# Performance work log

Hardware: AMD Instinct MI355X
Metric: run time of the kernel (lower is better)

Reference implementation:

```python
import jax, jax.numpy as jnp
import numpy as np

DIM = 96
EPS = 1e-5

def setup_inputs() -> dict:
    key = jax.random.key(0)
    k1, k2, k3, k4 = jax.random.split(key, 4)
    x = jax.random.normal(k1, (2, DIM, 32, 64, 64), dtype=jnp.float32)
    # LayerNorm(8*dim) params and Linear(8*dim -> 2*dim, bias=False) weight
    gamma = jnp.ones((8 * DIM,), dtype=jnp.float32)
    beta = jnp.zeros((8 * DIM,), dtype=jnp.float32)
    w_red = jax.random.normal(k2, (8 * DIM, 2 * DIM), dtype=jnp.float32) * (1.0 / np.sqrt(8 * DIM))
    return {"x": x, "gamma": gamma, "beta": beta, "w_red": w_red}


def _patch_merge(x, gamma, beta, w_red):
    B, C, D, H, W = x.shape
    # pad trailing spatial dims to even (static shapes -> python ifs are fine)
    if (D % 2) or (H % 2) or (W % 2):
        x = jnp.pad(x, ((0, 0), (0, 0), (0, D % 2), (0, H % 2), (0, W % 2)))
    x = jnp.transpose(x, (0, 2, 3, 4, 1))  # B, D, H, W, C
    # gather the 8 octant sub-lattices and concat on channel
    parts = [x[:, d::2, h::2, w::2, :]
             for d in (0, 1) for h in (0, 1) for w in (0, 1)]
    # torch order: x0..x7 indexed by (d,h,w) bits with d slowest -> matches loop order
    y = jnp.concatenate(parts, axis=-1)  # B, D/2, H/2, W/2, 8C
    # LayerNorm over last dim
    mu = jnp.mean(y, axis=-1, keepdims=True)
    var = jnp.mean(jnp.square(y - mu), axis=-1, keepdims=True)
    y = (y - mu) * jax.lax.rsqrt(var + EPS) * gamma + beta
    # Linear 8C -> 2C, no bias
    y = jnp.einsum('bdhwc,co->bdhwo', y, w_red)
    return jnp.transpose(y, (0, 4, 1, 2, 3))  # B, 2C, D/2, H/2, W/2


def reference(x, gamma, beta, w_red):
    return _patch_merge(x, gamma, beta, w_red)
```

## Files before the change

kernel.cpp:

```cpp
#include <hip/hip_runtime.h>

typedef __attribute__((ext_vector_type(8))) short short8;
typedef __attribute__((ext_vector_type(4))) float float4v;

__device__ __forceinline__ unsigned short f2bf(float f) {
  unsigned int u = __float_as_uint(f);
  u += 0x7fffu + ((u >> 16) & 1u);
  return (unsigned short)(u >> 16);
}
__device__ __forceinline__ float bf2f(unsigned short h) {
  return __uint_as_float(((unsigned int)h) << 16);
}

__global__ __launch_bounds__(256)
void prep_kernel(const float* __restrict__ w_red, const float* __restrict__ gamma,
                 const float* __restrict__ beta, unsigned short* __restrict__ w_bf,
                 float* __restrict__ colsum, float* __restrict__ bias) {
  const int n = blockIdx.x;
  const int t = threadIdx.x;
  float cs = 0.f, bs = 0.f;
#pragma unroll
  for (int j = 0; j < 3; ++j) {
    int kp = j * 256 + t;
    int ko = (kp & 7) * 96 + (kp >> 3);
    float w = w_red[(size_t)ko * 192 + n];
    unsigned short v = f2bf(gamma[ko] * w);
    w_bf[(size_t)n * 768 + kp] = v;
    cs += bf2f(v);
    bs += beta[ko] * w;
  }
#pragma unroll
  for (int off = 1; off < 64; off <<= 1) {
    cs += __shfl_xor(cs, off, 64);
    bs += __shfl_xor(bs, off, 64);
  }
  __shared__ float red[2][4];
  const int wave = t >> 6;
  if ((t & 63) == 0) { red[0][wave] = cs; red[1][wave] = bs; }
  __syncthreads();
  if (t == 0) {
    colsum[n] = red[0][0] + red[0][1] + red[0][2] + red[0][3];
    bias[n]   = red[1][0] + red[1][1] + red[1][2] + red[1][3];
  }
}

__global__ __launch_bounds__(256, 3)
void pm_kernel(const float* __restrict__ x, const unsigned short* __restrict__ w_bf,
               const float* __restrict__ colsum, const float* __restrict__ bias,
               float* __restrict__ out) {
  __shared__ __align__(16) unsigned short Y[32][776];
  __shared__ float4 part4[4][16];
  __shared__ float smu[32], srs[32];

  const int tid = threadIdx.x;
  const int bid = blockIdx.x;
  const int b  = bid >> 9;
  const int dz = (bid >> 5) & 15;
  const int hy = bid & 31;

  const float* xb = x + (size_t)b * 12582912u + (size_t)dz * 8192u + (size_t)hy * 128u;

  float sum0 = 0.f, sq0 = 0.f, sum1 = 0.f, sq1 = 0.f;
#pragma unroll
  for (int it = 0; it < 24; ++it) {
    int idx4 = it * 256 + tid;
    int r  = idx4 >> 4;
    int c  = r >> 2;
    int di = (r >> 1) & 1;
    int hi = r & 1;
    int w0 = (idx4 & 15) << 2;
    float4 v = *(const float4*)(xb + (size_t)c * 131072u + di * 4096 + hi * 64 + w0);
    int wx0 = (idx4 & 15) << 1;
    int k0  = c * 8 + di * 4 + hi * 2;
    unsigned int p01 = (unsigned int)f2bf(v.x) | ((unsigned int)f2bf(v.y) << 16);
    unsigned int p23 = (unsigned int)f2bf(v.z) | ((unsigned int)f2bf(v.w) << 16);
    *(unsigned int*)&Y[wx0][k0]     = p01;
    *(unsigned int*)&Y[wx0 + 1][k0] = p23;
    sum0 += v.x + v.y;  sq0 += v.x * v.x + v.y * v.y;
    sum1 += v.z + v.w;  sq1 += v.z * v.z + v.w * v.w;
  }
#pragma unroll
  for (int off = 16; off < 64; off <<= 1) {
    sum0 += __shfl_xor(sum0, off, 64);  sq0 += __shfl_xor(sq0, off, 64);
    sum1 += __shfl_xor(sum1, off, 64);  sq1 += __shfl_xor(sq1, off, 64);
  }
  const int lane = tid & 63;
  const int wave = tid >> 6;
  if (lane < 16) part4[wave][lane] = make_float4(sum0, sq0, sum1, sq1);
  __syncthreads();

  if (tid < 32) {
    int sp = tid >> 1, odd = tid & 1;
    float s = 0.f, q = 0.f;
#pragma unroll
    for (int w = 0; w < 4; ++w) {
      float4 p = part4[w][sp];
      s += odd ? p.z : p.x;
      q += odd ? p.w : p.y;
    }
    float mu  = s * (1.f / 768.f);
    float var = q * (1.f / 768.f) - mu * mu;
    smu[tid] = mu;
    srs[tid] = rsqrtf(var + 1e-5f);
  }

  const int lrow = lane & 15;
  const int lq   = lane >> 4;

  float4v acc[2][3];
#pragma unroll
  for (int i2 = 0; i2 < 2; ++i2)
#pragma unroll
    for (int j2 = 0; j2 < 3; ++j2)
#pragma unroll
      for (int r = 0; r < 4; ++r) acc[i2][j2][r] = 0.f;

  const unsigned short* wrow[3];
#pragma unroll
  for (int t3 = 0; t3 < 3; ++t3)
    wrow[t3] = w_bf + (size_t)((wave * 3 + t3) * 16 + lrow) * 768 + lq * 8;

  short8 bcur[3];
#pragma unroll
  for (int t3 = 0; t3 < 3; ++t3) bcur[t3] = *(const short8*)(wrow[t3]);

  for (int kc = 0; kc < 24; ++kc) {
    int kn = (kc < 23) ? kc + 1 : kc;
    short8 bnext[3];
#pragma unroll
    for (int t3 = 0; t3 < 3; ++t3) bnext[t3] = *(const short8*)(wrow[t3] + kn * 32);
    short8 a0 = *(const short8*)&Y[lrow][kc * 32 + lq * 8];
    short8 a1 = *(const short8*)&Y[16 + lrow][kc * 32 + lq * 8];
#pragma unroll
    for (int t3 = 0; t3 < 3; ++t3) {
      acc[0][t3] = __builtin_amdgcn_mfma_f32_16x16x32_bf16(a0, bcur[t3], acc[0][t3], 0, 0, 0);
      acc[1][t3] = __builtin_amdgcn_mfma_f32_16x16x32_bf16(a1, bcur[t3], acc[1][t3], 0, 0, 0);
    }
#pragma unroll
    for (int t3 = 0; t3 < 3; ++t3) bcur[t3] = bnext[t3];
  }

  __syncthreads();
  float* Cs = (float*)&Y[0][0];
#pragma unroll
  for (int t3 = 0; t3 < 3; ++t3) {
    int ng = (wave * 3 + t3) * 16 + lrow;
    float cs_n = colsum[ng];
    float bi_n = bias[ng];
#pragma unroll
    for (int mt = 0; mt < 2; ++mt)
#pragma unroll
      for (int r = 0; r < 4; ++r) {
        int m = mt * 16 + lq * 4 + r;
        float v = srs[m] * (acc[mt][t3][r] - smu[m] * cs_n) + bi_n;
        Cs[ng * 40 + m] = v;
      }
  }
  __syncthreads();

  float* ob = out + (size_t)b * 3145728u + (size_t)dz * 1024u + (size_t)hy * 32u;
#pragma unroll
  for (int it = 0; it < 6; ++it) {
    int idx4 = it * 256 + tid;
    int o  = idx4 >> 3;
    int wq = idx4 & 7;
    float4 vv = *(const float4*)&Cs[o * 40 + wq * 4];
    *(float4*)(ob + (size_t)o * 16384u + wq * 4) = vv;
  }
}

extern "C" void kernel_launch(void* const* d_in, const int* in_sizes, int n_in,
                              void* d_out, int out_size, void* d_ws, size_t ws_size,
                              hipStream_t stream) {
  const float* x     = (const float*)d_in[0];
  const float* gamma = (const float*)d_in[1];
  const float* beta  = (const float*)d_in[2];
  const float* w_red = (const float*)d_in[3];
  float* out = (float*)d_out;

  unsigned short* w_bf = (unsigned short*)d_ws;
  float* colsum = (float*)((char*)d_ws + 294912);
  float* bias   = colsum + 192;

  prep_kernel<<<dim3(192), dim3(256), 0, stream>>>(w_red, gamma, beta, w_bf, colsum, bias);
  pm_kernel<<<dim3(1024), dim3(256), 0, stream>>>(x, w_bf, colsum, bias, out);
}
```

Baseline: 204.6 us.

## Batch all x loads upfront and deepen weight prefetch to two stages

All 24 float4 loads of x are issued into registers before any conversion or LDS store, so their memory latency overlaps instead of being serialised. Weight fragments are now prefetched two k-steps ahead rather than one, and the first two stages are loaded before the statistics phase. The colsum and bias loads are also moved ahead of the barrier. The added live registers (96 floats for x plus extra short8 buffers) may hurt occupancy under the 3-blocks-per-SM launch bound.

```diff
diff --git a/kernel.cpp b/kernel.cpp
--- a/kernel.cpp
+++ b/kernel.cpp
@@ -60,32 +60,51 @@
 
   const float* xb = x + (size_t)b * 12582912u + (size_t)dz * 8192u + (size_t)hy * 128u;
 
+  const int r0 = tid >> 4;
+  const int c0 = r0 >> 2;
+  const int di = (r0 >> 1) & 1;
+  const int hi = r0 & 1;
+  const int w0 = (tid & 15) << 2;
+  const float* xp = xb + (size_t)c0 * 131072u + di * 4096 + hi * 64 + w0;
+
+  float4 v[24];
+#pragma unroll
+  for (int it = 0; it < 24; ++it)
+    v[it] = *(const float4*)(xp + (size_t)it * 524288u);
+
+  const int lane = tid & 63;
+  const int wave = tid >> 6;
+  const int lrow = lane & 15;
+  const int lq   = lane >> 4;
+  const unsigned short* wrow[3];
+#pragma unroll
+  for (int t3 = 0; t3 < 3; ++t3)
+    wrow[t3] = w_bf + (size_t)((wave * 3 + t3) * 16 + lrow) * 768 + lq * 8;
+  short8 b0[3], b1[3];
+#pragma unroll
+  for (int t3 = 0; t3 < 3; ++t3) b0[t3] = *(const short8*)(wrow[t3]);
+#pragma unroll
+  for (int t3 = 0; t3 < 3; ++t3) b1[t3] = *(const short8*)(wrow[t3] + 32);
+
+  const int wx0 = (tid & 15) << 1;
+  const int k00 = c0 * 8 + di * 4 + hi * 2;
   float sum0 = 0.f, sq0 = 0.f, sum1 = 0.f, sq1 = 0.f;
 #pragma unroll
   for (int it = 0; it < 24; ++it) {
-    int idx4 = it * 256 + tid;
-    int r  = idx4 >> 4;
-    int c  = r >> 2;
-    int di = (r >> 1) & 1;
-    int hi = r & 1;
-    int w0 = (idx4 & 15) << 2;
-    float4 v = *(const float4*)(xb + (size_t)c * 131072u + di * 4096 + hi * 64 + w0);
-    int wx0 = (idx4 & 15) << 1;
-    int k0  = c * 8 + di * 4 + hi * 2;
-    unsigned int p01 = (unsigned int)f2bf(v.x) | ((unsigned int)f2bf(v.y) << 16);
-    unsigned int p23 = (unsigned int)f2bf(v.z) | ((unsigned int)f2bf(v.w) << 16);
+    float4 vv = v[it];
+    unsigned int p01 = (unsigned int)f2bf(vv.x) | ((unsigned int)f2bf(vv.y) << 16);
+    unsigned int p23 = (unsigned int)f2bf(vv.z) | ((unsigned int)f2bf(vv.w) << 16);
+    int k0 = it * 32 + k00;
     *(unsigned int*)&Y[wx0][k0]     = p01;
     *(unsigned int*)&Y[wx0 + 1][k0] = p23;
-    sum0 += v.x + v.y;  sq0 += v.x * v.x + v.y * v.y;
-    sum1 += v.z + v.w;  sq1 += v.z * v.z + v.w * v.w;
+    sum0 += vv.x + vv.y;  sq0 += vv.x * vv.x + vv.y * vv.y;
+    sum1 += vv.z + vv.w;  sq1 += vv.z * vv.z + vv.w * vv.w;
   }
 #pragma unroll
   for (int off = 16; off < 64; off <<= 1) {
     sum0 += __shfl_xor(sum0, off, 64);  sq0 += __shfl_xor(sq0, off, 64);
     sum1 += __shfl_xor(sum1, off, 64);  sq1 += __shfl_xor(sq1, off, 64);
   }
-  const int lane = tid & 63;
-  const int wave = tid >> 6;
   if (lane < 16) part4[wave][lane] = make_float4(sum0, sq0, sum1, sq1);
   __syncthreads();
 
@@ -104,9 +123,6 @@
     srs[tid] = rsqrtf(var + 1e-5f);
   }
 
-  const int lrow = lane & 15;
-  const int lq   = lane >> 4;
-
   float4v acc[2][3];
 #pragma unroll
   for (int i2 = 0; i2 < 2; ++i2)
@@ -115,45 +131,42 @@
 #pragma unroll
       for (int r = 0; r < 4; ++r) acc[i2][j2][r] = 0.f;
 
-  const unsigned short* wrow[3];
-#pragma unroll
-  for (int t3 = 0; t3 < 3; ++t3)
-    wrow[t3] = w_bf + (size_t)((wave * 3 + t3) * 16 + lrow) * 768 + lq * 8;
-
-  short8 bcur[3];
-#pragma unroll
-  for (int t3 = 0; t3 < 3; ++t3) bcur[t3] = *(const short8*)(wrow[t3]);
-
   for (int kc = 0; kc < 24; ++kc) {
-    int kn = (kc < 23) ? kc + 1 : kc;
-    short8 bnext[3];
-#pragma unroll
-    for (int t3 = 0; t3 < 3; ++t3) bnext[t3] = *(const short8*)(wrow[t3] + kn * 32);
+    int kn = (kc + 2 <= 23) ? kc + 2 : 23;
+    short8 b2[3];
+#pragma unroll
+    for (int t3 = 0; t3 < 3; ++t3) b2[t3] = *(const short8*)(wrow[t3] + kn * 32);
     short8 a0 = *(const short8*)&Y[lrow][kc * 32 + lq * 8];
     short8 a1 = *(const short8*)&Y[16 + lrow][kc * 32 + lq * 8];
 #pragma unroll
     for (int t3 = 0; t3 < 3; ++t3) {
-      acc[0][t3] = __builtin_amdgcn_mfma_f32_16x16x32_bf16(a0, bcur[t3], acc[0][t3], 0, 0, 0);
-      acc[1][t3] = __builtin_amdgcn_mfma_f32_16x16x32_bf16(a1, bcur[t3], acc[1][t3], 0, 0, 0);
+      acc[0][t3] = __builtin_amdgcn_mfma_f32_16x16x32_bf16(a0, b0[t3], acc[0][t3], 0, 0, 0);
+      acc[1][t3] = __builtin_amdgcn_mfma_f32_16x16x32_bf16(a1, b0[t3], acc[1][t3], 0, 0, 0);
     }
 #pragma unroll
-    for (int t3 = 0; t3 < 3; ++t3) bcur[t3] = bnext[t3];
-  }
-
-  __syncthreads();
-  float* Cs = (float*)&Y[0][0];
+    for (int t3 = 0; t3 < 3; ++t3) { b0[t3] = b1[t3]; b1[t3] = b2[t3]; }
+  }
+
+  float cs_n[3], bi_n[3];
 #pragma unroll
   for (int t3 = 0; t3 < 3; ++t3) {
     int ng = (wave * 3 + t3) * 16 + lrow;
-    float cs_n = colsum[ng];
-    float bi_n = bias[ng];
+    cs_n[t3] = colsum[ng];
+    bi_n[t3] = bias[ng];
+  }
+
+  __syncthreads();
+  float* Cs = (float*)&Y[0][0];
+#pragma unroll
+  for (int t3 = 0; t3 < 3; ++t3) {
+    int ng = (wave * 3 + t3) * 16 + lrow;
 #pragma unroll
     for (int mt = 0; mt < 2; ++mt)
 #pragma unroll
       for (int r = 0; r < 4; ++r) {
         int m = mt * 16 + lq * 4 + r;
-        float v = srs[m] * (acc[mt][t3][r] - smu[m] * cs_n) + bi_n;
-        Cs[ng * 40 + m] = v;
+        float vv = srs[m] * (acc[mt][t3][r] - smu[m] * cs_n[t3]) + bi_n[t3];
+        Cs[ng * 40 + m] = vv;
       }
   }
   __syncthreads();
```

New measurement: 190.1 us. 1.08x faster.
